# Kernel tuning notes

Hardware: AMD Instinct MI355X
Metric: run time of the kernel (lower is better)

## Reference

```python
import jax, jax.numpy as jnp
import numpy as np
from jax import lax

N_C, N_P = 256, 32


def _fps(points, K):
    # farthest point sampling, deterministic start at index 0 (pytorch3d default)
    B, N, _ = points.shape
    idxs = jnp.zeros((B, K), dtype=jnp.int32)
    mind = jnp.sum((points - points[:, :1]) ** 2, axis=-1)  # [B,N]
    def body(i, carry):
        idxs, mind = carry
        far = jnp.argmax(mind, axis=1).astype(jnp.int32)  # [B]
        idxs = idxs.at[:, i].set(far)
        pf = jnp.take_along_axis(points, far[:, None, None], axis=1)  # [B,1,3]
        d = jnp.sum((points - pf) ** 2, axis=-1)
        return idxs, jnp.minimum(mind, d)
    idxs, _ = lax.fori_loop(1, K, body, (idxs, mind))
    return jnp.take_along_axis(points, idxs[..., None], axis=1)  # [B,K,3]


def _forward(data, perm, grid, We1, be1, We2, be2, Wf1a, bf1a, Wf1b, bf1b, Wf1c, bf1c,
             Wf2a, bf2a, Wf2b, bf2b, Wf2c, bf2c):
    pts = jnp.transpose(data, (0, 2, 1))  # [B,N,3]
    B = pts.shape[0]
    centers = lax.stop_gradient(_fps(pts, N_C))[:, perm]  # [B,N_C,3]
    # knn_points: squared distances centers->points, K nearest (sorted ascending)
    d = (jnp.sum(centers ** 2, -1)[..., None] + jnp.sum(pts ** 2, -1)[:, None, :]
         - 2.0 * jnp.einsum('bcd,bnd->bcn', centers, pts))  # [B,N_C,N]
    _, idx = lax.top_k(-d, N_P)  # [B,N_C,N_P]
    nn = jax.vmap(lambda p, i: p[i])(pts, idx)  # [B,N_C,N_P,3]
    center = nn.mean(axis=-2, keepdims=True)  # [B,N_C,1,3]
    local = nn - center
    scale = jnp.max(jnp.linalg.norm(local, axis=-1))  # global scalar
    local = local / scale
    x = local.reshape(-1, N_P, 3)  # [B*N_C, N_P, 3]
    # folding-net patch decoder
    h = jax.nn.relu(x @ We1 + be1)
    h = jax.nn.relu(h @ We2 + be2)
    code = h.max(axis=1)  # [M,256] codeword
    M = code.shape[0]
    codeb = jnp.broadcast_to(code[:, None, :], (M, N_P, code.shape[1]))
    g = jnp.broadcast_to(grid[None], (M, N_P, 2))
    f = jnp.concatenate([codeb, g], axis=-1)  # [M,N_P,258]
    f = jax.nn.relu(f @ Wf1a + bf1a)
    f = jax.nn.relu(f @ Wf1b + bf1b)
    f = f @ Wf1c + bf1c  # [M,N_P,3]
    f2 = jnp.concatenate([codeb, f], axis=-1)  # [M,N_P,259]
    f2 = jax.nn.relu(f2 @ Wf2a + bf2a)
    f2 = jax.nn.relu(f2 @ Wf2b + bf2b)
    f2 = f2 @ Wf2c + bf2c  # [M,N_P,3]
    return f2.reshape(B, N_C, N_P, 3) * scale + center


def setup_inputs() -> dict:
    key = jax.random.key(0)
    ks = jax.random.split(key, 20)
    w = lambda k, s: (jax.random.normal(k, s, dtype=jnp.float32) * 0.05)
    return {
        'data': jax.random.normal(ks[0], (32, 3, 8192), dtype=jnp.float32),
        'perm': jnp.arange(N_C, dtype=jnp.int32),
        'grid': jax.random.uniform(ks[1], (N_P, 2), dtype=jnp.float32),
        'We1': w(ks[2], (3, 128)), 'be1': w(ks[3], (128,)),
        'We2': w(ks[4], (128, 256)), 'be2': w(ks[5], (256,)),
        'Wf1a': w(ks[6], (258, 256)), 'bf1a': w(ks[7], (256,)),
        'Wf1b': w(ks[8], (256, 128)), 'bf1b': w(ks[9], (128,)),
        'Wf1c': w(ks[10], (128, 3)), 'bf1c': w(ks[11], (3,)),
        'Wf2a': w(ks[12], (259, 256)), 'bf2a': w(ks[13], (256,)),
        'Wf2b': w(ks[14], (256, 128)), 'bf2b': w(ks[15], (128,)),
        'Wf2c': w(ks[16], (128, 3)), 'bf2c': w(ks[17], (3,)),
    }


def reference(data, perm, grid, We1, be1, We2, be2, Wf1a, bf1a, Wf1b, bf1b, Wf1c, bf1c,
              Wf2a, bf2a, Wf2b, bf2b, Wf2c, bf2c):
    return _forward(data, perm, grid, We1, be1, We2, be2, Wf1a, bf1a, Wf1b, bf1b,
                    Wf1c, bf1c, Wf2a, bf2a, Wf2b, bf2b, Wf2c, bf2c)
```

## Files before the change

kernel.cpp:

```cpp
#include <hip/hip_runtime.h>

#define NB 32
#define NN 8192
#define NC 256
#define NP 32
#define MYFLT_MAX 3.402823466e+38f

typedef __attribute__((ext_vector_type(8))) short short8;
typedef __attribute__((ext_vector_type(4))) float f32x4;

__device__ __forceinline__ float b2f(unsigned short u) {
    return __uint_as_float(((unsigned)u) << 16);
}
__device__ __forceinline__ unsigned short f2b(float f) {
    unsigned u = __float_as_uint(f);
    unsigned r = u + 0x7fffu + ((u >> 16) & 1u);
    return (unsigned short)(r >> 16);
}
template<bool F32>
__device__ __forceinline__ float LD(const void* __restrict__ p, size_t i) {
    if (F32) return ((const float* __restrict__)p)[i];
    else     return b2f(((const unsigned short* __restrict__)p)[i]);
}
__device__ __forceinline__ float sq3(float x, float y, float z) {
    return __fadd_rn(__fadd_rn(__fmul_rn(x, x), __fmul_rn(y, y)), __fmul_rn(z, z));
}

template<int CTRL>
__device__ __forceinline__ void dpp_max2(unsigned& hi, unsigned& lo) {
    unsigned nh = (unsigned)__builtin_amdgcn_update_dpp(0, (int)hi, CTRL, 0xF, 0xF, true);
    unsigned nl = (unsigned)__builtin_amdgcn_update_dpp(0, (int)lo, CTRL, 0xF, 0xF, true);
    if (nh > hi || (nh == hi && nl > lo)) { hi = nh; lo = nl; }
}

__global__ void init_kernel(unsigned int* w) {
    w[0] = 0u;
    w[2] = 0u;
}

__global__ __launch_bounds__(256) void detect_kernel(
        const void* __restrict__ data, unsigned int* __restrict__ flag) {
    const unsigned short* u = (const unsigned short*)data;
    int t = blockIdx.x * 256 + threadIdx.x;
    unsigned cnt = 0;
    for (size_t i = (size_t)t * 2; i < 786432; i += 131072)
        if ((u[i] & 0x7F80u) == 0x7F80u) cnt++;
    if (cnt) atomicAdd(flag, cnt);
}

__device__ __forceinline__ size_t bfrag_idx(int k, int n, int nks) {
    int nt = n >> 4, ks = k >> 5;
    int lane = (n & 15) + 16 * ((k & 31) >> 3);
    return ((size_t)(nt * nks + ks) * 64 + lane) * 8 + (k & 7);
}
template<bool F32>
__global__ __launch_bounds__(256) void prep_kernel(
        const void* __restrict__ We2, const void* __restrict__ Wf1b,
        const void* __restrict__ Wf2b, const void* __restrict__ Wf1a,
        const void* __restrict__ Wf2a, const unsigned int* __restrict__ flagp,
        unsigned short* __restrict__ We2_sw, unsigned short* __restrict__ Wf1b_sw,
        unsigned short* __restrict__ Wf2b_sw, unsigned int* __restrict__ p1,
        unsigned int* __restrict__ p2) {
    if ((flagp[0] != 0u) != F32) return;
    int i = blockIdx.x * 256 + threadIdx.x;
    if (i < 32768) {
        int k = i >> 8, n = i & 255;
        We2_sw[bfrag_idx(k, n, 4)] = f2b(LD<F32>(We2, i));
    } else if (i < 65536) {
        int j = i - 32768, k = j >> 7, n = j & 127;
        Wf1b_sw[bfrag_idx(k, n, 8)] = f2b(LD<F32>(Wf1b, j));
    } else if (i < 98304) {
        int j = i - 65536, k = j >> 7, n = j & 127;
        Wf2b_sw[bfrag_idx(k, n, 8)] = f2b(LD<F32>(Wf2b, j));
    } else if (i < 131072) {
        int j = i - 98304, k2 = j >> 8, c = j & 255;
        unsigned lo = f2b(LD<F32>(Wf1a, (size_t)(2 * k2) * 256 + c));
        unsigned hi = f2b(LD<F32>(Wf1a, (size_t)(2 * k2 + 1) * 256 + c));
        p1[j] = lo | (hi << 16);
    } else {
        int j = i - 131072, k2 = j >> 8, c = j & 255;
        unsigned lo = f2b(LD<F32>(Wf2a, (size_t)(2 * k2) * 256 + c));
        unsigned hi = f2b(LD<F32>(Wf2a, (size_t)(2 * k2 + 1) * 256 + c));
        p2[j] = lo | (hi << 16);
    }
}

template<bool F32>
__global__ __launch_bounds__(1024) void fps_kernel(
        const void* __restrict__ data, const unsigned int* __restrict__ flagp,
        float* __restrict__ centers) {
    __shared__ unsigned rhi[16], rlo[16];
    __shared__ unsigned winlo_s;
    if ((flagp[0] != 0u) != F32) return;
    const int b = blockIdx.x, tid = threadIdx.x;
    const int lane = tid & 63;
    const size_t base = (size_t)b * 3 * NN;
    const float x0 = LD<F32>(data, base);
    const float y0 = LD<F32>(data, base + NN);
    const float z0 = LD<F32>(data, base + 2 * NN);
    float px[8], py[8], pz[8], mind[8];
#pragma unroll
    for (int j = 0; j < 8; j++) {
        int n = tid + 1024 * j;
        px[j] = LD<F32>(data, base + n);
        py[j] = LD<F32>(data, base + NN + n);
        pz[j] = LD<F32>(data, base + 2 * NN + n);
        mind[j] = sq3(__fsub_rn(px[j], x0), __fsub_rn(py[j], y0), __fsub_rn(pz[j], z0));
    }
    if (tid == 0) {
        centers[(b * NC + 0) * 3 + 0] = x0;
        centers[(b * NC + 0) * 3 + 1] = y0;
        centers[(b * NC + 0) * 3 + 2] = z0;
    }
    for (int i = 1; i < NC; i++) {
        unsigned hi = __float_as_uint(mind[0]);
        unsigned lo = ~(unsigned)tid;
#pragma unroll
        for (int j = 1; j < 8; j++) {
            unsigned h2 = __float_as_uint(mind[j]);
            unsigned l2 = ~(unsigned)(tid + 1024 * j);
            if (h2 > hi || (h2 == hi && l2 > lo)) { hi = h2; lo = l2; }
        }
        dpp_max2<0x111>(hi, lo);
        dpp_max2<0x112>(hi, lo);
        dpp_max2<0x114>(hi, lo);
        dpp_max2<0x118>(hi, lo);
        dpp_max2<0x142>(hi, lo);
        dpp_max2<0x143>(hi, lo);
        if (lane == 63) { rhi[tid >> 6] = hi; rlo[tid >> 6] = lo; }
        __syncthreads();
        if (tid < 64) {
            unsigned h = (tid < 16) ? rhi[tid] : 0u;
            unsigned l = (tid < 16) ? rlo[tid] : 0u;
            dpp_max2<0x111>(h, l);
            dpp_max2<0x112>(h, l);
            dpp_max2<0x114>(h, l);
            dpp_max2<0x118>(h, l);
            if (tid == 15) winlo_s = l;
        }
        __syncthreads();
        const int g = (int)(~winlo_s);
        const float cx = LD<F32>(data, base + g);
        const float cy = LD<F32>(data, base + NN + g);
        const float cz = LD<F32>(data, base + 2 * NN + g);
        if (tid == 0) {
            centers[(b * NC + i) * 3 + 0] = cx;
            centers[(b * NC + i) * 3 + 1] = cy;
            centers[(b * NC + i) * 3 + 2] = cz;
        }
#pragma unroll
        for (int j = 0; j < 8; j++) {
            float d = sq3(__fsub_rn(px[j], cx), __fsub_rn(py[j], cy), __fsub_rn(pz[j], cz));
            mind[j] = fminf(mind[j], d);
        }
    }
}

template<bool F32>
__global__ __launch_bounds__(256) void knn_kernel(
        const void* __restrict__ data, const int* __restrict__ perm,
        const float* __restrict__ centers, const unsigned int* __restrict__ flagp,
        unsigned int* __restrict__ scale_bits,
        int* __restrict__ selp, float* __restrict__ cmp) {
    __shared__ float dist[NN];
    __shared__ float rv4[4];
    __shared__ int   ri4[4];
    __shared__ int   winbuf;
    __shared__ int   sel[NP];
    if ((flagp[0] != 0u) != F32) return;
    const int m = blockIdx.x, b = m >> 8, c = m & 255, tid = threadIdx.x;
    const int ci = perm[c];
    const float cx = centers[((size_t)b * NC + ci) * 3 + 0];
    const float cy = centers[((size_t)b * NC + ci) * 3 + 1];
    const float cz = centers[((size_t)b * NC + ci) * 3 + 2];
    const float cn2 = sq3(cx, cy, cz);
    const size_t base = (size_t)b * 3 * NN;

    float bv = MYFLT_MAX; int bn = tid;
#pragma unroll 4
    for (int j = 0; j < 32; j++) {
        int n = tid + 256 * j;
        float x = LD<F32>(data, base + n);
        float y = LD<F32>(data, base + NN + n);
        float z = LD<F32>(data, base + 2 * NN + n);
        float pn2 = sq3(x, y, z);
        float dot = __fadd_rn(__fadd_rn(__fmul_rn(cx, x), __fmul_rn(cy, y)), __fmul_rn(cz, z));
        float d = __fsub_rn(__fadd_rn(cn2, pn2), __fmul_rn(2.0f, dot));
        dist[n] = d;
        if (d < bv) { bv = d; bn = n; }
    }
    for (int r = 0; r < NP; r++) {
        float v = bv; int n = bn;
#pragma unroll
        for (int off = 32; off >= 1; off >>= 1) {
            float ov = __shfl_down(v, off);
            int   on = __shfl_down(n, off);
            if (ov < v || (ov == v && on < n)) { v = ov; n = on; }
        }
        if ((tid & 63) == 0) { rv4[tid >> 6] = v; ri4[tid >> 6] = n; }
        __syncthreads();
        if (tid == 0) {
            float cv = rv4[0]; int cn = ri4[0];
#pragma unroll
            for (int w = 1; w < 4; w++)
                if (rv4[w] < cv || (rv4[w] == cv && ri4[w] < cn)) { cv = rv4[w]; cn = ri4[w]; }
            if ((unsigned)cn >= NN) cn = 0;
            winbuf = cn; sel[r] = cn;
        }
        __syncthreads();
        const int g = winbuf;
        if ((g & 255) == tid) {
            dist[g] = MYFLT_MAX;
            bv = MYFLT_MAX; bn = tid;
#pragma unroll 4
            for (int j = 0; j < 32; j++) {
                int nn2 = tid + 256 * j;
                float v2 = dist[nn2];
                if (v2 < bv) { bv = v2; bn = nn2; }
            }
        }
    }
    __syncthreads();
    if (tid < 32) {
        const int g = sel[tid];
        if (selp) selp[(size_t)m * 32 + tid] = g;
        float x = LD<F32>(data, base + g);
        float y = LD<F32>(data, base + NN + g);
        float z = LD<F32>(data, base + 2 * NN + g);
        float sx = x, sy = y, sz = z;
#pragma unroll
        for (int msk = 16; msk >= 1; msk >>= 1) {
            sx += __shfl_xor(sx, msk);
            sy += __shfl_xor(sy, msk);
            sz += __shfl_xor(sz, msk);
        }
        float mx = sx / 32.0f, my = sy / 32.0f, mz = sz / 32.0f;
        if (cmp && tid == 0) {
            cmp[(size_t)m * 3 + 0] = mx;
            cmp[(size_t)m * 3 + 1] = my;
            cmp[(size_t)m * 3 + 2] = mz;
        }
        float lx = x - mx, ly = y - my, lz = z - mz;
        float n2 = sq3(lx, ly, lz);
#pragma unroll
        for (int msk = 16; msk >= 1; msk >>= 1)
            n2 = fmaxf(n2, __shfl_xor(n2, msk));
        if (tid == 0) atomicMax(scale_bits, __float_as_uint(n2));
    }
}

__global__ void finalize_kernel(const unsigned int* scale_bits, float* scale_v) {
    scale_v[0] = sqrtf(__uint_as_float(scale_bits[0]));
}

__device__ __forceinline__ int afrag_idx(int p, int c) {
    int ks = c >> 5, mt = p >> 4;
    int lane = (p & 15) + 16 * ((c & 31) >> 3);
    return ((ks * 2 + mt) * 64 + lane) * 8 + (c & 7);
}

template<bool F32>
__global__ __launch_bounds__(256) void encdec_mfma(
        const void* __restrict__ data, const int* __restrict__ selp,
        const float* __restrict__ cmp, const float* __restrict__ scale_p,
        const unsigned int* __restrict__ flagp, const void* __restrict__ gridw,
        const void* __restrict__ We1, const void* __restrict__ be1,
        const unsigned short* __restrict__ We2_sw, const void* __restrict__ be2,
        const void* __restrict__ Wf1a, const unsigned int* __restrict__ p1,
        const void* __restrict__ bf1a,
        const unsigned short* __restrict__ Wf1b_sw, const void* __restrict__ bf1b,
        const void* __restrict__ Wf1c, const void* __restrict__ bf1c,
        const void* __restrict__ Wf2a, const unsigned int* __restrict__ p2,
        const void* __restrict__ bf2a,
        const unsigned short* __restrict__ Wf2b_sw, const void* __restrict__ bf2b,
        const void* __restrict__ Wf2c, const void* __restrict__ bf2c,
        void* __restrict__ out) {
    __shared__ unsigned short afrag[8192];
    __shared__ float g2s[32 * 132];
    __shared__ float code[256];
    __shared__ float xb[96];
    __shared__ float fb[96];
    __shared__ float gridb[64];
    if ((flagp[0] != 0u) != F32) return;
    const int m = blockIdx.x, b = m >> 8, tid = threadIdx.x;
    const int wv = tid >> 6, lane = tid & 63;
    const float scale = scale_p[0];
    const size_t base = (size_t)b * 3 * NN;
    if (tid < 64) gridb[tid] = LD<F32>(gridw, tid);
    if (tid < 32) {
        const int g = selp[(size_t)m * 32 + tid];
        xb[tid * 3 + 0] = (LD<F32>(data, base + g)          - cmp[(size_t)m * 3 + 0]) / scale;
        xb[tid * 3 + 1] = (LD<F32>(data, base + NN + g)     - cmp[(size_t)m * 3 + 1]) / scale;
        xb[tid * 3 + 2] = (LD<F32>(data, base + 2 * NN + g) - cmp[(size_t)m * 3 + 2]) / scale;
    }
    __syncthreads();
    for (int o = tid; o < 4096; o += 256) {
        int p = o >> 7, ch = o & 127;
        float v = xb[p * 3 + 0] * LD<F32>(We1, ch) + xb[p * 3 + 1] * LD<F32>(We1, 128 + ch)
                + xb[p * 3 + 2] * LD<F32>(We1, 256 + ch) + LD<F32>(be1, ch);
        afrag[afrag_idx(p, ch)] = f2b(fmaxf(v, 0.0f));
    }
    __syncthreads();
    {
        f32x4 acc[2][4];
#pragma unroll
        for (int a = 0; a < 2; a++)
#pragma unroll
            for (int t = 0; t < 4; t++) acc[a][t] = (f32x4){0.f, 0.f, 0.f, 0.f};
#pragma unroll
        for (int ks = 0; ks < 4; ks++) {
            short8 a0 = *(const short8*)&afrag[((ks * 2 + 0) * 64 + lane) * 8];
            short8 a1 = *(const short8*)&afrag[((ks * 2 + 1) * 64 + lane) * 8];
#pragma unroll
            for (int nt = 0; nt < 4; nt++) {
                short8 bf = *(const short8*)&We2_sw[((size_t)((4 * wv + nt) * 4 + ks) * 64 + lane) * 8];
                acc[0][nt] = __builtin_amdgcn_mfma_f32_16x16x32_bf16(a0, bf, acc[0][nt], 0, 0, 0);
                acc[1][nt] = __builtin_amdgcn_mfma_f32_16x16x32_bf16(a1, bf, acc[1][nt], 0, 0, 0);
            }
        }
#pragma unroll
        for (int nt = 0; nt < 4; nt++) {
            float mx = acc[0][nt][0];
#pragma unroll
            for (int r = 1; r < 4; r++) mx = fmaxf(mx, acc[0][nt][r]);
#pragma unroll
            for (int r = 0; r < 4; r++) mx = fmaxf(mx, acc[1][nt][r]);
            mx = fmaxf(mx, __shfl_xor(mx, 16));
            mx = fmaxf(mx, __shfl_xor(mx, 32));
            int n = 64 * wv + nt * 16 + (lane & 15);
            if (lane < 16) code[n] = fmaxf(mx + LD<F32>(be2, n), 0.0f);
        }
    }
    __syncthreads();
    {
        float a0 = 0.f, a1 = 0.f;
#pragma unroll 8
        for (int k2 = 0; k2 < 128; k2++) {
            unsigned u = p1[k2 * 256 + tid];
            a0 = fmaf(code[2 * k2],     b2f((unsigned short)(u & 0xffffu)), a0);
            a1 = fmaf(code[2 * k2 + 1], b2f((unsigned short)(u >> 16)), a1);
        }
        float base1 = a0 + a1 + LD<F32>(bf1a, tid);
        float wu = LD<F32>(Wf1a, 65536 + tid);
        float wvv = LD<F32>(Wf1a, 65792 + tid);
#pragma unroll 8
        for (int p = 0; p < 32; p++) {
            float v = base1 + gridb[2 * p] * wu + gridb[2 * p + 1] * wvv;
            afrag[afrag_idx(p, tid)] = f2b(fmaxf(v, 0.0f));
        }
    }
    __syncthreads();
    {
        f32x4 acc[2][2];
#pragma unroll
        for (int a = 0; a < 2; a++)
#pragma unroll
            for (int t = 0; t < 2; t++) acc[a][t] = (f32x4){0.f, 0.f, 0.f, 0.f};
#pragma unroll
        for (int ks = 0; ks < 8; ks++) {
            short8 a0 = *(const short8*)&afrag[((ks * 2 + 0) * 64 + lane) * 8];
            short8 a1 = *(const short8*)&afrag[((ks * 2 + 1) * 64 + lane) * 8];
#pragma unroll
            for (int nt = 0; nt < 2; nt++) {
                short8 bf = *(const short8*)&Wf1b_sw[((size_t)((2 * wv + nt) * 8 + ks) * 64 + lane) * 8];
                acc[0][nt] = __builtin_amdgcn_mfma_f32_16x16x32_bf16(a0, bf, acc[0][nt], 0, 0, 0);
                acc[1][nt] = __builtin_amdgcn_mfma_f32_16x16x32_bf16(a1, bf, acc[1][nt], 0, 0, 0);
            }
        }
#pragma unroll
        for (int nt = 0; nt < 2; nt++) {
            int n = 32 * wv + nt * 16 + (lane & 15);
            float bb = LD<F32>(bf1b, n);
#pragma unroll
            for (int mt = 0; mt < 2; mt++)
#pragma unroll
                for (int r = 0; r < 4; r++) {
                    int mm = mt * 16 + (lane >> 4) * 4 + r;
                    g2s[mm * 132 + n] = fmaxf(acc[mt][nt][r] + bb, 0.0f);
                }
        }
    }
    __syncthreads();
    if (tid < 96) {
        int p = tid / 3, e = tid % 3;
        float acc = 0.0f;
#pragma unroll 8
        for (int k = 0; k < 128; k++)
            acc = fmaf(g2s[p * 132 + k], LD<F32>(Wf1c, k * 3 + e), acc);
        fb[tid] = acc + LD<F32>(bf1c, e);
    }
    __syncthreads();
    {
        float a0 = 0.f, a1 = 0.f;
#pragma unroll 8
        for (int k2 = 0; k2 < 128; k2++) {
            unsigned u = p2[k2 * 256 + tid];
            a0 = fmaf(code[2 * k2],     b2f((unsigned short)(u & 0xffffu)), a0);
            a1 = fmaf(code[2 * k2 + 1], b2f((unsigned short)(u >> 16)), a1);
        }
        float base2 = a0 + a1 + LD<F32>(bf2a, tid);
        float w0 = LD<F32>(Wf2a, 65536 + tid);
        float w1 = LD<F32>(Wf2a, 65792 + tid);
        float w2 = LD<F32>(Wf2a, 66048 + tid);
#pragma unroll 8
        for (int p = 0; p < 32; p++) {
            float v = base2 + fb[p * 3] * w0 + fb[p * 3 + 1] * w1 + fb[p * 3 + 2] * w2;
            afrag[afrag_idx(p, tid)] = f2b(fmaxf(v, 0.0f));
        }
    }
    __syncthreads();
    {
        f32x4 acc[2][2];
#pragma unroll
        for (int a = 0; a < 2; a++)
#pragma unroll
            for (int t = 0; t < 2; t++) acc[a][t] = (f32x4){0.f, 0.f, 0.f, 0.f};
#pragma unroll
        for (int ks = 0; ks < 8; ks++) {
            short8 a0 = *(const short8*)&afrag[((ks * 2 + 0) * 64 + lane) * 8];
            short8 a1 = *(const short8*)&afrag[((ks * 2 + 1) * 64 + lane) * 8];
#pragma unroll
            for (int nt = 0; nt < 2; nt++) {
                short8 bf = *(const short8*)&Wf2b_sw[((size_t)((2 * wv + nt) * 8 + ks) * 64 + lane) * 8];
                acc[0][nt] = __builtin_amdgcn_mfma_f32_16x16x32_bf16(a0, bf, acc[0][nt], 0, 0, 0);
                acc[1][nt] = __builtin_amdgcn_mfma_f32_16x16x32_bf16(a1, bf, acc[1][nt], 0, 0, 0);
            }
        }
#pragma unroll
        for (int nt = 0; nt < 2; nt++) {
            int n = 32 * wv + nt * 16 + (lane & 15);
            float bb = LD<F32>(bf2b, n);
#pragma unroll
            for (int mt = 0; mt < 2; mt++)
#pragma unroll
                for (int r = 0; r < 4; r++) {
                    int mm = mt * 16 + (lane >> 4) * 4 + r;
                    g2s[mm * 132 + n] = fmaxf(acc[mt][nt][r] + bb, 0.0f);
                }
        }
    }
    __syncthreads();
    if (tid < 96) {
        int p = tid / 3, e = tid % 3;
        float acc = 0.0f;
#pragma unroll 8
        for (int k = 0; k < 128; k++)
            acc = fmaf(g2s[p * 132 + k], LD<F32>(Wf2c, k * 3 + e), acc);
        float v = (acc + LD<F32>(bf2c, e)) * scale + cmp[(size_t)m * 3 + e];
        size_t oi = (size_t)m * 96 + tid;
        if (F32) ((float*)out)[oi] = v;
        else     ((unsigned short*)out)[oi] = f2b(v);
    }
}

template<bool F32>
__global__ __launch_bounds__(256) void encdec_fused(
        const void* __restrict__ data,
        const int* __restrict__ perm, const float* __restrict__ centers,
        const float* __restrict__ scale_p, const unsigned int* __restrict__ flagp,
        const void* __restrict__ gridw,
        const void* __restrict__ We1, const void* __restrict__ be1,
        const void* __restrict__ We2, const void* __restrict__ be2,
        const void* __restrict__ Wf1a, const void* __restrict__ bf1a,
        const void* __restrict__ Wf1b, const void* __restrict__ bf1b,
        const void* __restrict__ Wf1c, const void* __restrict__ bf1c,
        const void* __restrict__ Wf2a, const void* __restrict__ bf2a,
        const void* __restrict__ Wf2b, const void* __restrict__ bf2b,
        const void* __restrict__ Wf2c, const void* __restrict__ bf2c,
        void* __restrict__ out) {
    __shared__ float bigA[256 * 36];
    __shared__ float bigB[128 * 36];
    __shared__ float code[256];
    __shared__ float xb[96];
    __shared__ float fb[96];
    __shared__ float gridb[64];
    __shared__ float meansh[4];
    __shared__ float rv4[4];
    __shared__ int   ri4[4];
    __shared__ int   winbuf;
    __shared__ int   sel[NP];
    if ((flagp[0] != 0u) != F32) return;
    const int m = (NB * NC - 1) - blockIdx.x;
    const int b = m >> 8, c = m & 255, tid = threadIdx.x;
    const float scale = scale_p[0];
    const int ci = perm[c];
    const float cx = centers[((size_t)b * NC + ci) * 3 + 0];
    const float cy = centers[((size_t)b * NC + ci) * 3 + 1];
    const float cz = centers[((size_t)b * NC + ci) * 3 + 2];
    const float cn2 = sq3(cx, cy, cz);
    const size_t base = (size_t)b * 3 * NN;
    if (tid < 64) gridb[tid] = LD<F32>(gridw, tid);
    float* dist = bigA;
    float bv = MYFLT_MAX; int bn = tid;
#pragma unroll 4
    for (int j = 0; j < 32; j++) {
        int n = tid + 256 * j;
        float x = LD<F32>(data, base + n);
        float y = LD<F32>(data, base + NN + n);
        float z = LD<F32>(data, base + 2 * NN + n);
        float pn2 = sq3(x, y, z);
        float dot = __fadd_rn(__fadd_rn(__fmul_rn(cx, x), __fmul_rn(cy, y)), __fmul_rn(cz, z));
        float d = __fsub_rn(__fadd_rn(cn2, pn2), __fmul_rn(2.0f, dot));
        dist[n] = d;
        if (d < bv) { bv = d; bn = n; }
    }
    for (int r = 0; r < NP; r++) {
        float v = bv; int n = bn;
#pragma unroll
        for (int off = 32; off >= 1; off >>= 1) {
            float ov = __shfl_down(v, off);
            int   on = __shfl_down(n, off);
            if (ov < v || (ov == v && on < n)) { v = ov; n = on; }
        }
        if ((tid & 63) == 0) { rv4[tid >> 6] = v; ri4[tid >> 6] = n; }
        __syncthreads();
        if (tid == 0) {
            float cv = rv4[0]; int cn = ri4[0];
#pragma unroll
            for (int w = 1; w < 4; w++)
                if (rv4[w] < cv || (rv4[w] == cv && ri4[w] < cn)) { cv = rv4[w]; cn = ri4[w]; }
            if ((unsigned)cn >= NN) cn = 0;
            winbuf = cn; sel[r] = cn;
        }
        __syncthreads();
        const int g = winbuf;
        if ((g & 255) == tid) {
            dist[g] = MYFLT_MAX;
            bv = MYFLT_MAX; bn = tid;
#pragma unroll 4
            for (int j = 0; j < 32; j++) {
                int nn2 = tid + 256 * j;
                float v2 = dist[nn2];
                if (v2 < bv) { bv = v2; bn = nn2; }
            }
        }
    }
    __syncthreads();
    if (tid < 32) {
        const int g = sel[tid];
        float x = LD<F32>(data, base + g);
        float y = LD<F32>(data, base + NN + g);
        float z = LD<F32>(data, base + 2 * NN + g);
        float sx = x, sy = y, sz = z;
#pragma unroll
        for (int msk = 16; msk >= 1; msk >>= 1) {
            sx += __shfl_xor(sx, msk);
            sy += __shfl_xor(sy, msk);
            sz += __shfl_xor(sz, msk);
        }
        float mx = sx / 32.0f, my = sy / 32.0f, mz = sz / 32.0f;
        xb[tid * 3 + 0] = (x - mx) / scale;
        xb[tid * 3 + 1] = (y - my) / scale;
        xb[tid * 3 + 2] = (z - mz) / scale;
        if (tid == 0) { meansh[0] = mx; meansh[1] = my; meansh[2] = mz; }
    }
    __syncthreads();
    for (int o = tid; o < 4096; o += 256) {
        int p = o >> 7, i = o & 127;
        float v = xb[p * 3 + 0] * LD<F32>(We1, i) + xb[p * 3 + 1] * LD<F32>(We1, 128 + i)
                + xb[p * 3 + 2] * LD<F32>(We1, 256 + i) + LD<F32>(be1, i);
        bigB[i * 36 + p] = fmaxf(v, 0.0f);
    }
    __syncthreads();
    {
        float acc[32];
#pragma unroll
        for (int p = 0; p < 32; p++) acc[p] = 0.0f;
        for (int k = 0; k < 128; k++) {
            float w = LD<F32>(We2, k * 256 + tid);
            const float4* hp = (const float4*)&bigB[k * 36];
#pragma unroll
            for (int q = 0; q < 8; q++) {
                float4 h4 = hp[q];
                acc[q * 4 + 0] = fmaf(h4.x, w, acc[q * 4 + 0]);
                acc[q * 4 + 1] = fmaf(h4.y, w, acc[q * 4 + 1]);
                acc[q * 4 + 2] = fmaf(h4.z, w, acc[q * 4 + 2]);
                acc[q * 4 + 3] = fmaf(h4.w, w, acc[q * 4 + 3]);
            }
        }
        float mx = acc[0];
#pragma unroll
        for (int p = 1; p < 32; p++) mx = fmaxf(mx, acc[p]);
        code[tid] = fmaxf(mx + LD<F32>(be2, tid), 0.0f);
    }
    __syncthreads();
    {
        float a0 = 0.f, a1 = 0.f, a2 = 0.f, a3 = 0.f;
        for (int k = 0; k < 256; k += 4) {
            a0 = fmaf(code[k + 0], LD<F32>(Wf1a, (k + 0) * 256 + tid), a0);
            a1 = fmaf(code[k + 1], LD<F32>(Wf1a, (k + 1) * 256 + tid), a1);
            a2 = fmaf(code[k + 2], LD<F32>(Wf1a, (k + 2) * 256 + tid), a2);
            a3 = fmaf(code[k + 3], LD<F32>(Wf1a, (k + 3) * 256 + tid), a3);
        }
        float base1 = ((a0 + a1) + (a2 + a3)) + LD<F32>(bf1a, tid);
        float wu = LD<F32>(Wf1a, 65536 + tid);
        float wvv = LD<F32>(Wf1a, 65792 + tid);
#pragma unroll 8
        for (int p = 0; p < 32; p++) {
            float v = base1 + gridb[2 * p] * wu + gridb[2 * p + 1] * wvv;
            bigA[tid * 36 + p] = fmaxf(v, 0.0f);
        }
    }
    __syncthreads();
    {
        int j = tid & 127, ph = tid >> 7;
        float acc[16];
#pragma unroll
        for (int q = 0; q < 16; q++) acc[q] = 0.0f;
        for (int k = 0; k < 256; k++) {
            float w = LD<F32>(Wf1b, k * 128 + j);
            const float4* gp = (const float4*)&bigA[k * 36 + ph * 16];
            float4 h0 = gp[0], h1 = gp[1], h2 = gp[2], h3 = gp[3];
            acc[0] = fmaf(h0.x, w, acc[0]);   acc[1] = fmaf(h0.y, w, acc[1]);
            acc[2] = fmaf(h0.z, w, acc[2]);   acc[3] = fmaf(h0.w, w, acc[3]);
            acc[4] = fmaf(h1.x, w, acc[4]);   acc[5] = fmaf(h1.y, w, acc[5]);
            acc[6] = fmaf(h1.z, w, acc[6]);   acc[7] = fmaf(h1.w, w, acc[7]);
            acc[8] = fmaf(h2.x, w, acc[8]);   acc[9] = fmaf(h2.y, w, acc[9]);
            acc[10] = fmaf(h2.z, w, acc[10]); acc[11] = fmaf(h2.w, w, acc[11]);
            acc[12] = fmaf(h3.x, w, acc[12]); acc[13] = fmaf(h3.y, w, acc[13]);
            acc[14] = fmaf(h3.z, w, acc[14]); acc[15] = fmaf(h3.w, w, acc[15]);
        }
        float bb = LD<F32>(bf1b, j);
#pragma unroll
        for (int q = 0; q < 16; q++)
            bigB[j * 36 + ph * 16 + q] = fmaxf(acc[q] + bb, 0.0f);
    }
    __syncthreads();
    if (tid < 96) {
        int p = tid / 3, e = tid % 3;
        float acc = 0.0f;
        for (int k = 0; k < 128; k++)
            acc = fmaf(bigB[k * 36 + p], LD<F32>(Wf1c, k * 3 + e), acc);
        fb[tid] = acc + LD<F32>(bf1c, e);
    }
    __syncthreads();
    {
        float a0 = 0.f, a1 = 0.f, a2 = 0.f, a3 = 0.f;
        for (int k = 0; k < 256; k += 4) {
            a0 = fmaf(code[k + 0], LD<F32>(Wf2a, (k + 0) * 256 + tid), a0);
            a1 = fmaf(code[k + 1], LD<F32>(Wf2a, (k + 1) * 256 + tid), a1);
            a2 = fmaf(code[k + 2], LD<F32>(Wf2a, (k + 2) * 256 + tid), a2);
            a3 = fmaf(code[k + 3], LD<F32>(Wf2a, (k + 3) * 256 + tid), a3);
        }
        float base2 = ((a0 + a1) + (a2 + a3)) + LD<F32>(bf2a, tid);
        float w0 = LD<F32>(Wf2a, 65536 + tid);
        float w1 = LD<F32>(Wf2a, 65792 + tid);
        float w2 = LD<F32>(Wf2a, 66048 + tid);
#pragma unroll 8
        for (int p = 0; p < 32; p++) {
            float v = base2 + fb[p * 3] * w0 + fb[p * 3 + 1] * w1 + fb[p * 3 + 2] * w2;
            bigA[tid * 36 + p] = fmaxf(v, 0.0f);
        }
    }
    __syncthreads();
    {
        int j = tid & 127, ph = tid >> 7;
        float acc[16];
#pragma unroll
        for (int q = 0; q < 16; q++) acc[q] = 0.0f;
        for (int k = 0; k < 256; k++) {
            float w = LD<F32>(Wf2b, k * 128 + j);
            const float4* gp = (const float4*)&bigA[k * 36 + ph * 16];
            float4 h0 = gp[0], h1 = gp[1], h2 = gp[2], h3 = gp[3];
            acc[0] = fmaf(h0.x, w, acc[0]);   acc[1] = fmaf(h0.y, w, acc[1]);
            acc[2] = fmaf(h0.z, w, acc[2]);   acc[3] = fmaf(h0.w, w, acc[3]);
            acc[4] = fmaf(h1.x, w, acc[4]);   acc[5] = fmaf(h1.y, w, acc[5]);
            acc[6] = fmaf(h1.z, w, acc[6]);   acc[7] = fmaf(h1.w, w, acc[7]);
            acc[8] = fmaf(h2.x, w, acc[8]);   acc[9] = fmaf(h2.y, w, acc[9]);
            acc[10] = fmaf(h2.z, w, acc[10]); acc[11] = fmaf(h2.w, w, acc[11]);
            acc[12] = fmaf(h3.x, w, acc[12]); acc[13] = fmaf(h3.y, w, acc[13]);
            acc[14] = fmaf(h3.z, w, acc[14]); acc[15] = fmaf(h3.w, w, acc[15]);
        }
        float bb = LD<F32>(bf2b, j);
#pragma unroll
        for (int q = 0; q < 16; q++)
            bigB[j * 36 + ph * 16 + q] = fmaxf(acc[q] + bb, 0.0f);
    }
    __syncthreads();
    if (tid < 96) {
        int p = tid / 3, e = tid % 3;
        float acc = 0.0f;
        for (int k = 0; k < 128; k++)
            acc = fmaf(bigB[k * 36 + p], LD<F32>(Wf2c, k * 3 + e), acc);
        float v = (acc + LD<F32>(bf2c, e)) * scale + meansh[e];
        size_t oi = (size_t)m * 96 + tid;
        if (F32) ((float*)out)[oi] = v;
        else     ((unsigned short*)out)[oi] = f2b(v);
    }
}

extern "C" void kernel_launch(void* const* d_in, const int* in_sizes, int n_in,
                              void* d_out, int out_size, void* d_ws, size_t ws_size,
                              hipStream_t stream) {
    const void* data = d_in[0];
    const int* perm  = (const int*)d_in[1];
    const void* grid = d_in[2];
    const void *We1 = d_in[3], *be1 = d_in[4], *We2 = d_in[5], *be2 = d_in[6];
    const void *Wf1a = d_in[7], *bf1a = d_in[8], *Wf1b = d_in[9], *bf1b = d_in[10];
    const void *Wf1c = d_in[11], *bf1c = d_in[12];
    const void *Wf2a = d_in[13], *bf2a = d_in[14], *Wf2b = d_in[15], *bf2b = d_in[16];
    const void *Wf2c = d_in[17], *bf2c = d_in[18];

    if (ws_size >= (size_t)4 * 1024 * 1024) {
        float* ws = (float*)d_ws;
        unsigned int* wbase   = (unsigned int*)ws;
        float*        scale_v = ws + 1;
        unsigned int* flagp   = wbase + 2;
        float*        centers = ws + 4;
        float*        cmeanp  = ws + 24580;
        int*          selp    = (int*)(ws + 49156);
        unsigned short* We2_sw  = (unsigned short*)(ws + 311304);
        unsigned short* Wf1b_sw = (unsigned short*)(ws + 327688);
        unsigned short* Wf2b_sw = (unsigned short*)(ws + 344072);
        unsigned int*   p1      = (unsigned int*)(ws + 360456);
        unsigned int*   p2      = (unsigned int*)(ws + 393224);

        init_kernel<<<1, 1, 0, stream>>>(wbase);
        detect_kernel<<<256, 256, 0, stream>>>(data, flagp);
        prep_kernel<false><<<640, 256, 0, stream>>>(We2, Wf1b, Wf2b, Wf1a, Wf2a, flagp,
                                                    We2_sw, Wf1b_sw, Wf2b_sw, p1, p2);
        prep_kernel<true ><<<640, 256, 0, stream>>>(We2, Wf1b, Wf2b, Wf1a, Wf2a, flagp,
                                                    We2_sw, Wf1b_sw, Wf2b_sw, p1, p2);
        fps_kernel<false><<<NB, 1024, 0, stream>>>(data, flagp, centers);
        fps_kernel<true ><<<NB, 1024, 0, stream>>>(data, flagp, centers);
        knn_kernel<false><<<NB * NC, 256, 0, stream>>>(data, perm, centers, flagp, wbase, selp, cmeanp);
        knn_kernel<true ><<<NB * NC, 256, 0, stream>>>(data, perm, centers, flagp, wbase, selp, cmeanp);
        finalize_kernel<<<1, 1, 0, stream>>>(wbase, scale_v);
        encdec_mfma<false><<<NB * NC, 256, 0, stream>>>(data, selp, cmeanp, scale_v, flagp, grid,
                We1, be1, We2_sw, be2, Wf1a, p1, bf1a, Wf1b_sw, bf1b, Wf1c, bf1c,
                Wf2a, p2, bf2a, Wf2b_sw, bf2b, Wf2c, bf2c, d_out);
        encdec_mfma<true ><<<NB * NC, 256, 0, stream>>>(data, selp, cmeanp, scale_v, flagp, grid,
                We1, be1, We2_sw, be2, Wf1a, p1, bf1a, Wf1b_sw, bf1b, Wf1c, bf1c,
                Wf2a, p2, bf2a, Wf2b_sw, bf2b, Wf2c, bf2c, d_out);
    } else {
        float* ov = (ws_size >= (size_t)131072) ? (float*)d_ws : (float*)d_out;
        unsigned int* wbase   = (unsigned int*)ov;
        float*        scale_v = ov + 1;
        unsigned int* flagp   = wbase + 2;
        float*        centers = ov + 4;

        init_kernel<<<1, 1, 0, stream>>>(wbase);
        detect_kernel<<<256, 256, 0, stream>>>(data, flagp);
        fps_kernel<false><<<NB, 1024, 0, stream>>>(data, flagp, centers);
        fps_kernel<true ><<<NB, 1024, 0, stream>>>(data, flagp, centers);
        knn_kernel<false><<<NB * NC, 256, 0, stream>>>(data, perm, centers, flagp, wbase, nullptr, nullptr);
        knn_kernel<true ><<<NB * NC, 256, 0, stream>>>(data, perm, centers, flagp, wbase, nullptr, nullptr);
        finalize_kernel<<<1, 1, 0, stream>>>(wbase, scale_v);
        encdec_fused<false><<<NB * NC, 256, 0, stream>>>(data, perm, centers, scale_v, flagp,
                grid, We1, be1, We2, be2, Wf1a, bf1a, Wf1b, bf1b, Wf1c, bf1c,
                Wf2a, bf2a, Wf2b, bf2b, Wf2c, bf2c, d_out);
        encdec_fused<true ><<<NB * NC, 256, 0, stream>>>(data, perm, centers, scale_v, flagp,
                grid, We1, be1, We2, be2, Wf1a, bf1a, Wf1b, bf1b, Wf1c, bf1c,
                Wf2a, bf2a, Wf2b, bf2b, Wf2c, bf2c, d_out);
    }
}
```

Before: 1.205 ms.

## Keep kNN distances in registers and use DPP argmax reduction

Replaces the 32 KB shared-memory distance array in the kNN kernel with 32 per-thread register keys, encoded as order-preserving unsigned integers, plus a bitmask of removed entries. The per-round wave reduction moves from shuffles to DPP row/broadcast operations on (key, inverted index) pairs, and the cross-wave step runs on one wave with DPP instead of a serial loop in thread 0. This removes the LDS traffic and frees LDS so more blocks can be resident per CU, at the cost of higher VGPR pressure from the 32-entry register array.

```diff
diff --git a/kernel.cpp b/kernel.cpp
--- a/kernel.cpp
+++ b/kernel.cpp
@@ -24,6 +24,10 @@
 }
 __device__ __forceinline__ float sq3(float x, float y, float z) {
     return __fadd_rn(__fadd_rn(__fmul_rn(x, x), __fmul_rn(y, y)), __fmul_rn(z, z));
+}
+__device__ __forceinline__ unsigned mono(float f) {
+    unsigned u = __float_as_uint(f);
+    return (u & 0x80000000u) ? ~u : (u ^ 0x80000000u);
 }
 
 template<int CTRL>
@@ -162,13 +166,12 @@
         const float* __restrict__ centers, const unsigned int* __restrict__ flagp,
         unsigned int* __restrict__ scale_bits,
         int* __restrict__ selp, float* __restrict__ cmp) {
-    __shared__ float dist[NN];
-    __shared__ float rv4[4];
-    __shared__ int   ri4[4];
-    __shared__ int   winbuf;
-    __shared__ int   sel[NP];
+    __shared__ unsigned rhi4[4], rlo4[4];
+    __shared__ unsigned winlo_s;
+    __shared__ int sel[NP];
     if ((flagp[0] != 0u) != F32) return;
     const int m = blockIdx.x, b = m >> 8, c = m & 255, tid = threadIdx.x;
+    const int lane = tid & 63, wv = tid >> 6;
     const int ci = perm[c];
     const float cx = centers[((size_t)b * NC + ci) * 3 + 0];
     const float cy = centers[((size_t)b * NC + ci) * 3 + 1];
@@ -176,8 +179,9 @@
     const float cn2 = sq3(cx, cy, cz);
     const size_t base = (size_t)b * 3 * NN;
 
-    float bv = MYFLT_MAX; int bn = tid;
-#pragma unroll 4
+    unsigned kh[32];
+    unsigned bhi = 0u, blo = 0u;
+#pragma unroll
     for (int j = 0; j < 32; j++) {
         int n = tid + 256 * j;
         float x = LD<F32>(data, base + n);
@@ -186,37 +190,38 @@
         float pn2 = sq3(x, y, z);
         float dot = __fadd_rn(__fadd_rn(__fmul_rn(cx, x), __fmul_rn(cy, y)), __fmul_rn(cz, z));
         float d = __fsub_rn(__fadd_rn(cn2, pn2), __fmul_rn(2.0f, dot));
-        dist[n] = d;
-        if (d < bv) { bv = d; bn = n; }
-    }
+        kh[j] = ~mono(d);
+        unsigned l2 = ~(unsigned)n;
+        if (kh[j] > bhi || (kh[j] == bhi && l2 > blo)) { bhi = kh[j]; blo = l2; }
+    }
+    unsigned removed = 0u;
     for (int r = 0; r < NP; r++) {
-        float v = bv; int n = bn;
-#pragma unroll
-        for (int off = 32; off >= 1; off >>= 1) {
-            float ov = __shfl_down(v, off);
-            int   on = __shfl_down(n, off);
-            if (ov < v || (ov == v && on < n)) { v = ov; n = on; }
-        }
-        if ((tid & 63) == 0) { rv4[tid >> 6] = v; ri4[tid >> 6] = n; }
+        unsigned hi = bhi, lo = blo;
+        dpp_max2<0x111>(hi, lo);
+        dpp_max2<0x112>(hi, lo);
+        dpp_max2<0x114>(hi, lo);
+        dpp_max2<0x118>(hi, lo);
+        dpp_max2<0x142>(hi, lo);
+        dpp_max2<0x143>(hi, lo);
+        if (lane == 63) { rhi4[wv] = hi; rlo4[wv] = lo; }
         __syncthreads();
-        if (tid == 0) {
-            float cv = rv4[0]; int cn = ri4[0];
-#pragma unroll
-            for (int w = 1; w < 4; w++)
-                if (rv4[w] < cv || (rv4[w] == cv && ri4[w] < cn)) { cv = rv4[w]; cn = ri4[w]; }
-            if ((unsigned)cn >= NN) cn = 0;
-            winbuf = cn; sel[r] = cn;
+        if (tid < 64) {
+            unsigned h = (tid < 4) ? rhi4[tid] : 0u;
+            unsigned l = (tid < 4) ? rlo4[tid] : 0u;
+            dpp_max2<0x111>(h, l);
+            dpp_max2<0x112>(h, l);
+            if (tid == 3) { winlo_s = l; sel[r] = (int)~l; }
         }
         __syncthreads();
-        const int g = winbuf;
+        const int g = (int)(~winlo_s);
         if ((g & 255) == tid) {
-            dist[g] = MYFLT_MAX;
-            bv = MYFLT_MAX; bn = tid;
-#pragma unroll 4
+            removed |= 1u << (g >> 8);
+            bhi = 0u; blo = 0u;
+#pragma unroll
             for (int j = 0; j < 32; j++) {
-                int nn2 = tid + 256 * j;
-                float v2 = dist[nn2];
-                if (v2 < bv) { bv = v2; bn = nn2; }
+                unsigned h2 = ((removed >> j) & 1u) ? 0u : kh[j];
+                unsigned l2 = ~(unsigned)(tid + 256 * j);
+                if (h2 > bhi || (h2 == bhi && l2 > blo)) { bhi = h2; blo = l2; }
             }
         }
     }
```

After: 1.292 ms. 7.2% more time.
